# Performance work log

Hardware: AMD Instinct MI355X
Metric: run time of the kernel (lower is better)

Reference implementation:

```python
import jax, jax.numpy as jnp
import numpy as np

B, N, H = 2048, 5, 5
IN, HID, OUT = 7, 2048, 512  # IN = 1 + c + c^2 with c = (H-1)//2 = 2


def setup_inputs() -> dict:
    key = jax.random.key(0)
    ks = jax.random.split(key, 7)
    k_in = 1.0 / np.sqrt(IN).astype(np.float32)
    k_h = 1.0 / np.sqrt(HID).astype(np.float32)
    return {
        "ins": jax.random.normal(ks[0], (B, N, H, H), jnp.float32),
        "w1": (jax.random.uniform(ks[1], (4, HID, IN), jnp.float32) - 0.5) * k_in,
        "b1": (jax.random.uniform(ks[2], (HID,), jnp.float32) - 0.5) * k_in,
        "w2": (jax.random.uniform(ks[3], (4, HID, HID), jnp.float32) - 0.5) * k_h,
        "b2": (jax.random.uniform(ks[4], (HID,), jnp.float32) - 0.5) * k_h,
        "w3": (jax.random.uniform(ks[5], (4, OUT, HID), jnp.float32) - 0.5) * k_h,
        "b3": (jax.random.uniform(ks[6], (OUT,), jnp.float32) - 0.5) * k_h,
        "ln_g": jnp.ones((HID,), jnp.float32),
        "ln_b": jnp.zeros((HID,), jnp.float32),
    }


def _rot90(x):
    # matches torch: x.flip(3).permute(0,1,3,2)
    return jnp.swapaxes(jnp.flip(x, axis=3), 2, 3)


def _orbit_stack(x):
    b, n = x.shape[0], x.shape[1]
    c = (x.shape[-1] - 1) // 2  # = 2 for H=5
    center = x[:, :, c, c]  # (B,N)
    parts = []
    xi = x
    for _ in range(4):  # fixed C4 group orbit, not a data loop
        parts.append(xi[:, :, :c, :c + 1].reshape(b, n, -1))  # (B,N,c+c^2)
        xi = _rot90(xi)
    orb = jnp.stack(parts, axis=-1)  # (B,N,c+c^2,4)
    cen = jnp.broadcast_to(center[..., None, None], (b, n, 1, 4))
    out = jnp.concatenate([cen, orb], axis=2)  # (B,N,n_orbits,4)
    return jnp.transpose(out, (0, 1, 3, 2))  # (B,N,4,n_orbits)


def _c4conv(w, bias, x):
    # block-circulant kernel: mat[g,h] = w[(h-g) % 4]
    mat = jnp.stack([jnp.roll(w, i, axis=0) for i in range(4)], axis=0)  # (4,4,out,in)
    return jnp.einsum('ghij,bnhj->bngi', mat, x) + bias


def _layernorm(x, g, b, eps=1e-5):
    m = jnp.mean(x, axis=-1, keepdims=True)
    v = jnp.mean(jnp.square(x - m), axis=-1, keepdims=True)
    return (x - m) / jnp.sqrt(v + eps) * g + b


def reference(ins, w1, b1, w2, b2, w3, b3, ln_g, ln_b):
    h = _orbit_stack(ins)                          # (B,N,4,7)
    h = jax.nn.relu(_c4conv(w1, b1, h))            # (B,N,4,HID)
    h = jax.nn.relu(_layernorm(_c4conv(w2, b2, h), ln_g, ln_b))
    return _c4conv(w3, b3, h)                      # (B,N,4,OUT)
```

## Files before the change

### kernel.cpp

```cpp
#include <hip/hip_runtime.h>
#include <stdint.h>


#define HID 2048
#define MROWS 10240

typedef float floatx4 __attribute__((ext_vector_type(4)));
typedef __bf16 bf16x8 __attribute__((ext_vector_type(8)));

__device__ __forceinline__ unsigned short f2bf(float f) {
  union { float f; unsigned int u; } v; v.f = f;
  unsigned int r = v.u + 0x7fffu + ((v.u >> 16) & 1u);
  return (unsigned short)(r >> 16);
}
__device__ __forceinline__ float bf2f(unsigned short s) {
  union { unsigned int u; float f; } v; v.u = ((unsigned int)s) << 16;
  return v.f;
}

template <int NO>
__global__ __launch_bounds__(256) void wtrans_kernel(const float* __restrict__ w,
                                                     unsigned short* __restrict__ W0s,
                                                     unsigned short* __restrict__ W2s,
                                                     unsigned short* __restrict__ Bc) {
  int idx = blockIdx.x * 256 + threadIdx.x;
  int i = idx >> 9, j4 = idx & 511;
  const float4* wp = (const float4*)w;
  float4 w0 = wp[0 * NO * 512 + i * 512 + j4];
  float4 w1 = wp[1 * NO * 512 + i * 512 + j4];
  float4 w2 = wp[2 * NO * 512 + i * 512 + j4];
  float4 w3 = wp[3 * NO * 512 + i * 512 + j4];
  ushort4 s0, s2, vr, vi, nvi;
#define DO(c)                                        \
  s0.c = f2bf(w0.c + w1.c + w2.c + w3.c);            \
  s2.c = f2bf(w0.c - w1.c + w2.c - w3.c);            \
  vr.c = f2bf(w0.c - w2.c);                          \
  vi.c = f2bf(w1.c - w3.c);                          \
  nvi.c = f2bf(-(w1.c - w3.c));
  DO(x) DO(y) DO(z) DO(w)
#undef DO
  ((ushort4*)W0s)[i * 512 + j4] = s0;
  ((ushort4*)W2s)[i * 512 + j4] = s2;
  ((ushort4*)Bc)[i * 1024 + j4] = vr;
  ((ushort4*)Bc)[i * 1024 + 512 + j4] = nvi;
  ((ushort4*)Bc)[(NO + i) * 1024 + j4] = vi;
  ((ushort4*)Bc)[(NO + i) * 1024 + 512 + j4] = vr;
}

__global__ __launch_bounds__(256) void layer1_kernel(const float* __restrict__ ins,
                                                     const float* __restrict__ w1,
                                                     const float* __restrict__ b1,
                                                     unsigned short* __restrict__ h1s,
                                                     int row0) {
  __shared__ float orbs[32][28];
  int t = threadIdx.x;
  int b0 = blockIdx.x * 32;
  int i = blockIdx.y * 256 + t;
  if (t < 32) {
    const float* x = ins + (size_t)(row0 + b0 + t) * 25;
    float v[25];
#pragma unroll
    for (int p = 0; p < 25; ++p) v[p] = x[p];
    float* o = orbs[t];
    o[0] = v[12]; o[7] = v[12]; o[14] = v[12]; o[21] = v[12];
#pragma unroll
    for (int r = 0; r < 2; ++r)
#pragma unroll
      for (int c = 0; c < 3; ++c) {
        int m = 1 + r * 3 + c;
        o[m]      = v[r * 5 + c];
        o[7 + m]  = v[c * 5 + (4 - r)];
        o[14 + m] = v[(4 - r) * 5 + (4 - c)];
        o[21 + m] = v[(4 - c) * 5 + r];
      }
  }
  __syncthreads();
  float w[4][7];
#pragma unroll
  for (int r = 0; r < 4; ++r)
#pragma unroll
    for (int j = 0; j < 7; ++j) w[r][j] = w1[(r * HID + i) * 7 + j];
  float bias = b1[i];
  for (int s = 0; s < 32; ++s) {
    float a[4] = {bias, bias, bias, bias};
#pragma unroll
    for (int hh = 0; hh < 4; ++hh)
#pragma unroll
      for (int j = 0; j < 7; ++j) {
        float ov = orbs[s][hh * 7 + j];
#pragma unroll
        for (int g = 0; g < 4; ++g) a[g] += w[(hh - g) & 3][j] * ov;
      }
    float h0 = fmaxf(a[0], 0.f), h1 = fmaxf(a[1], 0.f);
    float h2 = fmaxf(a[2], 0.f), h3 = fmaxf(a[3], 0.f);
    size_t base = (size_t)(b0 + s) * 8192 + i;
    h1s[base]        = f2bf(h0 + h1 + h2 + h3);
    h1s[base + 2048] = f2bf(h0 - h1 + h2 - h3);
    h1s[base + 4096] = f2bf(h0 - h2);
    h1s[base + 6144] = f2bf(h3 - h1);
  }
}


__global__ __launch_bounds__(512, 2) void gemm_spec(const unsigned short* __restrict__ A,
                                                    const unsigned short* __restrict__ B0,
                                                    const unsigned short* __restrict__ B1,
                                                    const unsigned short* __restrict__ B2,
                                                    float* __restrict__ Cf,
                                                    unsigned short* __restrict__ Cb,
                                                    int s1, int s2, int N0, int ldc,
                                                    int NT, int NTL, int MTN) {
  __shared__ __align__(16) unsigned short As[2][16384];
  __shared__ __align__(16) unsigned short Bs[2][16384];
  int tid = threadIdx.x;
  int wave = tid >> 6, lane = tid & 63;
  int lane15 = lane & 15, lane4 = lane >> 4, l7 = lane15 & 7;
  int wm = wave >> 2, wn = wave & 3;
  int wm64 = wm << 6, wn32 = wn << 5;

  int srow = tid >> 3;
  int scol = ((tid & 7) ^ ((tid >> 3) & 7)) << 3;
  int bs64 = (srow >> 5) << 6;

#define STA(buf, mh, kk)                                                                              \
  __builtin_amdgcn_global_load_lds(                                                                   \
      (const __attribute__((address_space(1))) void*)(Agb + (size_t)((mh) * 64) * 8192 + (kk)),       \
      (__attribute__((address_space(3))) void*)((char*)As[buf] + (mh) * 16384 + wave * 1024),         \
      16, 0, 0);                                                                                      \
  __builtin_amdgcn_global_load_lds(                                                                   \
      (const __attribute__((address_space(1))) void*)(Agb + (size_t)((mh) * 64 + 128) * 8192 + (kk)), \
      (__attribute__((address_space(3))) void*)((char*)As[buf] + (mh) * 16384 + 8192 + wave * 1024),  \
      16, 0, 0)

#define STB(buf, nh, kk)                                                                              \
  __builtin_amdgcn_global_load_lds(                                                                   \
      (const __attribute__((address_space(1))) void*)(Bgb + (size_t)(bs64 + (nh) * 32) * ldb + (kk)), \
      (__attribute__((address_space(3))) void*)((char*)Bs[buf] + (nh) * 16384 + wave * 1024),         \
      16, 0, 0);                                                                                      \
  __builtin_amdgcn_global_load_lds(                                                                   \
      (const __attribute__((address_space(1))) void*)(Bgb + (size_t)(bs64 + 128 + (nh) * 32) * ldb + (kk)), \
      (__attribute__((address_space(3))) void*)((char*)Bs[buf] + (nh) * 16384 + 8192 + wave * 1024),  \
      16, 0, 0)

#define RAF(buf, mh)                                                                                  \
  _Pragma("unroll") for (int mi_ = 0; mi_ < 4; ++mi_)                                                 \
  _Pragma("unroll") for (int ks_ = 0; ks_ < 2; ++ks_)                                                 \
      af[mi_][ks_] = *(const bf16x8*)((const char*)As[buf] +                                          \
          (((mh) * 128 + wm64 + mi_ * 16 + lane15) << 7) + (((ks_ * 4 + lane4) ^ l7) << 4))

#define RBF(dst, buf, nh)                                                                             \
  _Pragma("unroll") for (int ni_ = 0; ni_ < 2; ++ni_)                                                 \
  _Pragma("unroll") for (int ks_ = 0; ks_ < 2; ++ks_)                                                 \
      dst[ni_][ks_] = *(const bf16x8*)((const char*)Bs[buf] +                                         \
          (((nh) * 128 + wn32 + ni_ * 16 + lane15) << 7) + (((ks_ * 4 + lane4) ^ l7) << 4))

#define MM(mh, nh, bF)                                                                                \
  _Pragma("unroll") for (int mi_ = 0; mi_ < 4; ++mi_)                                                 \
  _Pragma("unroll") for (int ni_ = 0; ni_ < 2; ++ni_)                                                 \
  _Pragma("unroll") for (int ks_ = 0; ks_ < 2; ++ks_)                                                 \
      acc[(mh) * 4 + mi_][(nh) * 2 + ni_] = __builtin_amdgcn_mfma_f32_16x16x32_bf16(                  \
          af[mi_][ks_], bF[ni_][ks_], acc[(mh) * 4 + mi_][(nh) * 2 + ni_], 0, 0, 0)

#define BAR() __builtin_amdgcn_s_barrier()
#define LGKM0() asm volatile("s_waitcnt lgkmcnt(0)" ::: "memory")
#define LGKM8() asm volatile("s_waitcnt lgkmcnt(8)" ::: "memory")
#define VM6() asm volatile("s_waitcnt vmcnt(6)" ::: "memory")
#define VM8() asm volatile("s_waitcnt vmcnt(8)" ::: "memory")

  bf16x8 af[4][2], b0r[2][2], b1r[2][2];
  const floatx4 fz = {0.f, 0.f, 0.f, 0.f};
  floatx4 acc[8][4];

  int G = (int)gridDim.x;
  for (int pass = 0;; ++pass) {
    int base = pass * G;
    if (base >= NT) break;
    int wt = (pass & 1) ? (base + G - 1 - (int)blockIdx.x) : (base + (int)blockIdx.x);
    if (wt >= NT) continue;

    int mt, nt;
    if (wt < NTL) { int j = wt / MTN; nt = s2 + j; mt = wt - j * MTN; }
    else          { int w2_ = wt - NTL; int j = w2_ / MTN; nt = j; mt = w2_ - j * MTN; }
    int m0 = mt * 256;

    const unsigned short* Bp;
    int K, aoff, coff, nloc;
    if (nt < s1)      { Bp = B0; K = 2048; aoff = 0;    coff = 0;      nloc = nt * 256; }
    else if (nt < s2) { Bp = B1; K = 2048; aoff = 2048; coff = N0;     nloc = (nt - s1) * 256; }
    else              { Bp = B2; K = 4096; aoff = 4096; coff = 2 * N0; nloc = (nt - s2) * 256; }
    int ldb = K;

    const unsigned short* Agb = A + (size_t)(m0 + srow) * 8192 + aoff + scol;
    const unsigned short* Bgb = Bp + (size_t)(nloc + (srow & 31)) * ldb + scol;

#pragma unroll
    for (int a = 0; a < 8; ++a)
#pragma unroll
      for (int b = 0; b < 4; ++b) acc[a][b] = fz;

    STA(0, 0, 0); STB(0, 0, 0); STB(0, 1, 0); STA(0, 1, 0);
    STA(1, 0, 64); STB(1, 0, 64); STB(1, 1, 64); STA(1, 1, 64);
    VM8();
    BAR();

    for (int k0 = 0; k0 < K; k0 += 128) {
      RAF(0, 0); RBF(b0r, 0, 0);
      LGKM8();
      BAR(); LGKM0();
      __builtin_amdgcn_s_setprio(1); MM(0, 0, b0r); __builtin_amdgcn_s_setprio(0);
      BAR();
      RBF(b1r, 0, 1);
      STA(0, 0, k0 + 128);
      BAR(); LGKM0();
      __builtin_amdgcn_s_setprio(1); MM(0, 1, b1r); __builtin_amdgcn_s_setprio(0);
      BAR();
      RAF(0, 1);
      STB(0, 0, k0 + 128);
      BAR(); LGKM0();
      __builtin_amdgcn_s_setprio(1); MM(1, 0, b0r); __builtin_amdgcn_s_setprio(0);
      BAR();
      STB(0, 1, k0 + 128);
      BAR(); LGKM0();
      __builtin_amdgcn_s_setprio(1); MM(1, 1, b1r); __builtin_amdgcn_s_setprio(0);
      VM6();
      BAR();
      RAF(1, 0); RBF(b0r, 1, 0);
      STA(0, 1, k0 + 128);
      LGKM8();
      BAR(); LGKM0();
      __builtin_amdgcn_s_setprio(1); MM(0, 0, b0r); __builtin_amdgcn_s_setprio(0);
      BAR();
      RBF(b1r, 1, 1);
      STA(1, 0, k0 + 192);
      BAR(); LGKM0();
      __builtin_amdgcn_s_setprio(1); MM(0, 1, b1r); __builtin_amdgcn_s_setprio(0);
      BAR();
      RAF(1, 1);
      STB(1, 0, k0 + 192);
      BAR(); LGKM0();
      __builtin_amdgcn_s_setprio(1); MM(1, 0, b0r); __builtin_amdgcn_s_setprio(0);
      BAR();
      STB(1, 1, k0 + 192);
      STA(1, 1, k0 + 192);
      BAR(); LGKM0();
      __builtin_amdgcn_s_setprio(1); MM(1, 1, b1r); __builtin_amdgcn_s_setprio(0);
      VM6();
      BAR();
    }
    asm volatile("s_waitcnt vmcnt(0)" ::: "memory");

#pragma unroll
    for (int ni = 0; ni < 4; ++ni) {
      int col = coff + nloc + wn * 64 + (ni >> 1) * 32 + (ni & 1) * 16 + lane15;
#pragma unroll
      for (int mi = 0; mi < 8; ++mi) {
        int row = m0 + wm * 128 + (mi >> 2) * 64 + (mi & 3) * 16 + lane4 * 4;
        if (Cb) {
#pragma unroll
          for (int r = 0; r < 4; ++r)
            __builtin_nontemporal_store(f2bf(acc[mi][ni][r]),
                                        &Cb[(size_t)(row + r) * ldc + col]);
        } else {
#pragma unroll
          for (int r = 0; r < 4; ++r)
            __builtin_nontemporal_store(acc[mi][ni][r],
                                        &Cf[(size_t)(row + r) * ldc + col]);
        }
      }
    }
  }
#undef STA
#undef STB
#undef RAF
#undef RBF
#undef MM
#undef BAR
#undef LGKM0
#undef LGKM8
#undef VM6
#undef VM8
}

__global__ __launch_bounds__(256) void ln_spec_kernel(const unsigned short* C2,
                                                      const float* __restrict__ b2,
                                                      const float* __restrict__ ln_g,
                                                      const float* __restrict__ ln_b,
                                                      unsigned short* h1s) {
  int t = threadIdx.x;
  size_t base = (size_t)blockIdx.x * 8192;
  const ushort4* p = (const ushort4*)(C2 + base);
  const float4* bp2 = (const float4*)b2;
  float4 y[4][2];
  float s[4] = {0, 0, 0, 0}, q[4] = {0, 0, 0, 0};
#pragma unroll
  for (int hl = 0; hl < 2; ++hl) {
    int j = hl * 256 + t;
    ushort4 u0 = p[j], u2 = p[512 + j], ur = p[1024 + j], ui = p[1536 + j];
    float4 bb = bp2[j];
#define DO(c)                                                   \
  {                                                             \
    float v0 = bf2f(u0.c), v2 = bf2f(u2.c);                     \
    float vr = bf2f(ur.c), vi = bf2f(ui.c);                     \
    float e0 = 0.25f * (v0 + v2 + 2.f * vr) + bb.c;             \
    float e1 = 0.25f * (v0 - v2 - 2.f * vi) + bb.c;             \
    float e2 = 0.25f * (v0 + v2 - 2.f * vr) + bb.c;             \
    float e3 = 0.25f * (v0 - v2 + 2.f * vi) + bb.c;             \
    y[0][hl].c = e0; y[1][hl].c = e1; y[2][hl].c = e2; y[3][hl].c = e3; \
    s[0] += e0; q[0] += e0 * e0; s[1] += e1; q[1] += e1 * e1;   \
    s[2] += e2; q[2] += e2 * e2; s[3] += e3; q[3] += e3 * e3;   \
  }
    DO(x) DO(y) DO(z) DO(w)
#undef DO
  }
#pragma unroll
  for (int off = 32; off > 0; off >>= 1)
#pragma unroll
    for (int g = 0; g < 4; ++g) {
      s[g] += __shfl_down(s[g], off, 64);
      q[g] += __shfl_down(q[g], off, 64);
    }
  __shared__ float rs[4][4], rq[4][4];
  int w = t >> 6, l = t & 63;
  if (l == 0)
#pragma unroll
    for (int g = 0; g < 4; ++g) { rs[w][g] = s[g]; rq[w][g] = q[g]; }
  __syncthreads();
  float mean[4], rstd[4];
#pragma unroll
  for (int g = 0; g < 4; ++g) {
    float ss = rs[0][g] + rs[1][g] + rs[2][g] + rs[3][g];
    float qq = rq[0][g] + rq[1][g] + rq[2][g] + rq[3][g];
    mean[g] = ss * (1.f / HID);
    float var = qq * (1.f / HID) - mean[g] * mean[g];
    rstd[g] = rsqrtf(var + 1e-5f);
  }
  const float4* gp = (const float4*)ln_g;
  const float4* lbp = (const float4*)ln_b;
#pragma unroll
  for (int hl = 0; hl < 2; ++hl) {
    int j = hl * 256 + t;
    float4 gg = gp[j], lb = lbp[j];
    ushort4 o[4];
#define DO(c)                                                               \
  {                                                                         \
    float h0 = fmaxf((y[0][hl].c - mean[0]) * rstd[0] * gg.c + lb.c, 0.f);  \
    float h1 = fmaxf((y[1][hl].c - mean[1]) * rstd[1] * gg.c + lb.c, 0.f);  \
    float h2 = fmaxf((y[2][hl].c - mean[2]) * rstd[2] * gg.c + lb.c, 0.f);  \
    float h3 = fmaxf((y[3][hl].c - mean[3]) * rstd[3] * gg.c + lb.c, 0.f);  \
    o[0].c = f2bf(h0 + h1 + h2 + h3);                                       \
    o[1].c = f2bf(h0 - h1 + h2 - h3);                                       \
    o[2].c = f2bf(h0 - h2);                                                 \
    o[3].c = f2bf(h3 - h1);                                                 \
  }
    DO(x) DO(y) DO(z) DO(w)
#undef DO
    size_t ob = (size_t)blockIdx.x * 8192;
#pragma unroll
    for (int pl = 0; pl < 4; ++pl)
      ((ushort4*)(h1s + ob + pl * 2048))[j] = o[pl];
  }
}

__global__ __launch_bounds__(256) void out_ep_kernel(const float* __restrict__ Z,
                                                     const float* __restrict__ b3,
                                                     float* __restrict__ out) {
  int e = blockIdx.x * 256 + threadIdx.x;
  int row = e >> 7, i4 = e & 127;
  const float4* Z4 = (const float4*)Z;
  const float4* b34 = (const float4*)b3;
  float4* o4 = (float4*)out;
  size_t base = (size_t)row * 512;
  float4 z0 = Z4[base + i4],       z2 = Z4[base + 128 + i4];
  float4 zr = Z4[base + 256 + i4], zi = Z4[base + 384 + i4];
  float4 bv = b34[i4];
  float4 e0, e1, e2, e3;
#define DO(c)                                     \
  e0.c = 0.25f * (z0.c + z2.c + 2.f * zr.c) + bv.c; \
  e1.c = 0.25f * (z0.c - z2.c - 2.f * zi.c) + bv.c; \
  e2.c = 0.25f * (z0.c + z2.c - 2.f * zr.c) + bv.c; \
  e3.c = 0.25f * (z0.c - z2.c + 2.f * zi.c) + bv.c;
  DO(x) DO(y) DO(z) DO(w)
#undef DO
  o4[base + i4]       = e0;
  o4[base + 128 + i4] = e1;
  o4[base + 256 + i4] = e2;
  o4[base + 384 + i4] = e3;
}

extern "C" void kernel_launch(void* const* d_in, const int* in_sizes, int n_in,
                              void* d_out, int out_size, void* d_ws, size_t ws_size,
                              hipStream_t stream) {
  const float* ins = (const float*)d_in[0];
  const float* w1  = (const float*)d_in[1];
  const float* b1  = (const float*)d_in[2];
  const float* w2  = (const float*)d_in[3];
  const float* b2  = (const float*)d_in[4];
  const float* w3  = (const float*)d_in[5];
  const float* b3  = (const float*)d_in[6];
  const float* lng = (const float*)d_in[7];
  const float* lnb = (const float*)d_in[8];
  float* out = (float*)d_out;
  char* ws = (char*)d_ws;

  unsigned short* W0s2 = (unsigned short*)ws;
  unsigned short* W2s2 = W0s2 + 4194304;
  unsigned short* Bc2  = W2s2 + 4194304;
  unsigned short* W0s3 = Bc2 + 16777216;
  unsigned short* W2s3 = W0s3 + 1048576;
  unsigned short* Bc3  = W2s3 + 1048576;
  const size_t WT_BYTES = 62914560ull;
  char* chunk_base = ws + WT_BYTES;

  wtrans_kernel<2048><<<4096, 256, 0, stream>>>(w2, W0s2, W2s2, Bc2);
  wtrans_kernel<512><<<1024, 256, 0, stream>>>(w3, W0s3, W2s3, Bc3);

  const size_t H1_BYTES = (size_t)5120 * 8192 * 2;
  const size_t H2_BYTES = (size_t)MROWS * 8192 * 2;
  const size_t need_full = WT_BYTES + H1_BYTES + H2_BYTES + 4096;

  if (ws_size >= need_full) {
    unsigned short* h1s = (unsigned short*)chunk_base;
    float*          Z   = (float*)chunk_base;
    unsigned short* H2  = (unsigned short*)(chunk_base + H1_BYTES);
    const int Mc = 5120, MTN = Mc / 256;
    for (int c = 0; c < 2; ++c) {
      int row0 = c * Mc;
      unsigned short* H2c = H2 + (size_t)row0 * 8192;
      layer1_kernel<<<dim3(Mc / 32, 8), 256, 0, stream>>>(ins, w1, b1, h1s, row0);
      gemm_spec<<<256, 512, 0, stream>>>(h1s, W0s2, W2s2, Bc2, nullptr, H2c,
                                         8, 16, 2048, 8192, 32 * MTN, 16 * MTN, MTN);
      ln_spec_kernel<<<Mc, 256, 0, stream>>>(H2c, b2, lng, lnb, H2c);
    }
    {
      const int MT3 = MROWS / 256;
      gemm_spec<<<256, 512, 0, stream>>>(H2, W0s3, W2s3, Bc3, Z, nullptr,
                                         2, 4, 512, 2048, 8 * MT3, 4 * MT3, MT3);
      out_ep_kernel<<<MROWS / 2, 256, 0, stream>>>(Z, b3, out);
    }
  } else {
    static const int Pcand[8] = {1, 2, 4, 5, 8, 10, 20, 40};
    int P = 40;
    for (int pi = 0; pi < 8; ++pi) {
      size_t mc = (size_t)MROWS / Pcand[pi];
      size_t need = WT_BYTES + mc * 8192 * 2 * 2 + 4096;
      if (need <= ws_size) { P = Pcand[pi]; break; }
    }
    const int Mc = MROWS / P, MTN = Mc / 256;
    unsigned short* h1s = (unsigned short*)chunk_base;
    unsigned short* C2  = (unsigned short*)(chunk_base + (size_t)Mc * 8192 * 2);
    float*          Z   = (float*)C2;
    for (int c = 0; c < P; ++c) {
      int row0 = c * Mc;
      layer1_kernel<<<dim3(Mc / 32, 8), 256, 0, stream>>>(ins, w1, b1, h1s, row0);
      gemm_spec<<<256, 512, 0, stream>>>(h1s, W0s2, W2s2, Bc2, nullptr, C2,
                                         8, 16, 2048, 8192, 32 * MTN, 16 * MTN, MTN);
      ln_spec_kernel<<<Mc, 256, 0, stream>>>(C2, b2, lng, lnb, h1s);
      gemm_spec<<<256, 512, 0, stream>>>(h1s, W0s3, W2s3, Bc3, Z, nullptr,
                                         2, 4, 512, 2048, 8 * MTN, 4 * MTN, MTN);
      out_ep_kernel<<<Mc / 2, 256, 0, stream>>>(Z, b3, out + (size_t)row0 * 2048);
    }
  }
}
```

Baseline: 1.107 ms.

## Use Karatsuba-style complex product to cut C4 spectral GEMM work

The complex-frequency block of each C4 conv was a K=4096 real GEMM. It now uses three K=2048 real products (vr, vi, vr+vi) via a Karatsuba-style trick, and the real and imaginary parts are rebuilt in the LN and output epilogues. This cuts the FLOPs of the complex part from 4 to 3 real products, at the cost of a wider activation layout (AW=10240) and an extra stored plane. It also simplifies GEMM tile scheduling into uniform K=2048 segments, drops nontemporal stores, and switches the row chunking to 6144/4096 with layer 3 run per chunk.

```diff
diff --git a/kernel.cpp b/kernel.cpp
--- a/kernel.cpp
+++ b/kernel.cpp
@@ -4,6 +4,7 @@
 
 #define HID 2048
 #define MROWS 10240
+#define AW 10240
 
 typedef float floatx4 __attribute__((ext_vector_type(4)));
 typedef __bf16 bf16x8 __attribute__((ext_vector_type(8)));
@@ -20,9 +21,7 @@
 
 template <int NO>
 __global__ __launch_bounds__(256) void wtrans_kernel(const float* __restrict__ w,
-                                                     unsigned short* __restrict__ W0s,
-                                                     unsigned short* __restrict__ W2s,
-                                                     unsigned short* __restrict__ Bc) {
+                                                     unsigned short* __restrict__ Wb) {
   int idx = blockIdx.x * 256 + threadIdx.x;
   int i = idx >> 9, j4 = idx & 511;
   const float4* wp = (const float4*)w;
@@ -30,21 +29,25 @@
   float4 w1 = wp[1 * NO * 512 + i * 512 + j4];
   float4 w2 = wp[2 * NO * 512 + i * 512 + j4];
   float4 w3 = wp[3 * NO * 512 + i * 512 + j4];
-  ushort4 s0, s2, vr, vi, nvi;
+  ushort4 s0, s2, vr, vi, vs;
 #define DO(c)                                        \
-  s0.c = f2bf(w0.c + w1.c + w2.c + w3.c);            \
-  s2.c = f2bf(w0.c - w1.c + w2.c - w3.c);            \
-  vr.c = f2bf(w0.c - w2.c);                          \
-  vi.c = f2bf(w1.c - w3.c);                          \
-  nvi.c = f2bf(-(w1.c - w3.c));
+  {                                                  \
+    float vrf = w0.c - w2.c, vif = w1.c - w3.c;      \
+    s0.c = f2bf(w0.c + w1.c + w2.c + w3.c);          \
+    s2.c = f2bf(w0.c - w1.c + w2.c - w3.c);          \
+    vr.c = f2bf(vrf);                                \
+    vi.c = f2bf(vif);                                \
+    vs.c = f2bf(vrf + vif);                          \
+  }
   DO(x) DO(y) DO(z) DO(w)
 #undef DO
-  ((ushort4*)W0s)[i * 512 + j4] = s0;
-  ((ushort4*)W2s)[i * 512 + j4] = s2;
-  ((ushort4*)Bc)[i * 1024 + j4] = vr;
-  ((ushort4*)Bc)[i * 1024 + 512 + j4] = nvi;
-  ((ushort4*)Bc)[(NO + i) * 1024 + j4] = vi;
-  ((ushort4*)Bc)[(NO + i) * 1024 + 512 + j4] = vr;
+  ushort4* O = (ushort4*)Wb;
+  const int MS = NO * 512;
+  O[0 * MS + i * 512 + j4] = s0;
+  O[1 * MS + i * 512 + j4] = s2;
+  O[2 * MS + i * 512 + j4] = vr;
+  O[3 * MS + i * 512 + j4] = vi;
+  O[4 * MS + i * 512 + j4] = vs;
 }
 
 __global__ __launch_bounds__(256) void layer1_kernel(const float* __restrict__ ins,
@@ -93,23 +96,23 @@
       }
     float h0 = fmaxf(a[0], 0.f), h1 = fmaxf(a[1], 0.f);
     float h2 = fmaxf(a[2], 0.f), h3 = fmaxf(a[3], 0.f);
-    size_t base = (size_t)(b0 + s) * 8192 + i;
+    float ur = h0 - h2, ui = h3 - h1;
+    size_t base = (size_t)(b0 + s) * AW + i;
     h1s[base]        = f2bf(h0 + h1 + h2 + h3);
     h1s[base + 2048] = f2bf(h0 - h1 + h2 - h3);
-    h1s[base + 4096] = f2bf(h0 - h2);
-    h1s[base + 6144] = f2bf(h3 - h1);
+    h1s[base + 4096] = f2bf(ur);
+    h1s[base + 6144] = f2bf(ui);
+    h1s[base + 8192] = f2bf(ur + ui);
   }
 }
 
 
 __global__ __launch_bounds__(512, 2) void gemm_spec(const unsigned short* __restrict__ A,
-                                                    const unsigned short* __restrict__ B0,
-                                                    const unsigned short* __restrict__ B1,
-                                                    const unsigned short* __restrict__ B2,
+                                                    const unsigned short* __restrict__ Bb,
                                                     float* __restrict__ Cf,
                                                     unsigned short* __restrict__ Cb,
-                                                    int s1, int s2, int N0, int ldc,
-                                                    int NT, int NTL, int MTN) {
+                                                    int N0, int ldc,
+                                                    int NT, int MTN, int segN) {
   __shared__ __align__(16) unsigned short As[2][16384];
   __shared__ __align__(16) unsigned short Bs[2][16384];
   int tid = threadIdx.x;
@@ -121,14 +124,15 @@
   int srow = tid >> 3;
   int scol = ((tid & 7) ^ ((tid >> 3) & 7)) << 3;
   int bs64 = (srow >> 5) << 6;
+  const int K = 2048, ldb = 2048;
 
 #define STA(buf, mh, kk)                                                                              \
   __builtin_amdgcn_global_load_lds(                                                                   \
-      (const __attribute__((address_space(1))) void*)(Agb + (size_t)((mh) * 64) * 8192 + (kk)),       \
+      (const __attribute__((address_space(1))) void*)(Agb + (size_t)((mh) * 64) * AW + (kk)),         \
       (__attribute__((address_space(3))) void*)((char*)As[buf] + (mh) * 16384 + wave * 1024),         \
       16, 0, 0);                                                                                      \
   __builtin_amdgcn_global_load_lds(                                                                   \
-      (const __attribute__((address_space(1))) void*)(Agb + (size_t)((mh) * 64 + 128) * 8192 + (kk)), \
+      (const __attribute__((address_space(1))) void*)(Agb + (size_t)((mh) * 64 + 128) * AW + (kk)),   \
       (__attribute__((address_space(3))) void*)((char*)As[buf] + (mh) * 16384 + 8192 + wave * 1024),  \
       16, 0, 0)
 
@@ -178,19 +182,13 @@
     int wt = (pass & 1) ? (base + G - 1 - (int)blockIdx.x) : (base + (int)blockIdx.x);
     if (wt >= NT) continue;
 
-    int mt, nt;
-    if (wt < NTL) { int j = wt / MTN; nt = s2 + j; mt = wt - j * MTN; }
-    else          { int w2_ = wt - NTL; int j = w2_ / MTN; nt = j; mt = w2_ - j * MTN; }
+    int nt = wt / MTN, mt = wt - nt * MTN;
     int m0 = mt * 256;
-
-    const unsigned short* Bp;
-    int K, aoff, coff, nloc;
-    if (nt < s1)      { Bp = B0; K = 2048; aoff = 0;    coff = 0;      nloc = nt * 256; }
-    else if (nt < s2) { Bp = B1; K = 2048; aoff = 2048; coff = N0;     nloc = (nt - s1) * 256; }
-    else              { Bp = B2; K = 4096; aoff = 4096; coff = 2 * N0; nloc = (nt - s2) * 256; }
-    int ldb = K;
-
-    const unsigned short* Agb = A + (size_t)(m0 + srow) * 8192 + aoff + scol;
+    int seg = nt / segN, nloc = (nt - seg * segN) * 256;
+    const unsigned short* Bp = Bb + (size_t)seg * N0 * 2048;
+    int aoff = seg * 2048, coff = seg * N0;
+
+    const unsigned short* Agb = A + (size_t)(m0 + srow) * AW + aoff + scol;
     const unsigned short* Bgb = Bp + (size_t)(nloc + (srow & 31)) * ldb + scol;
 
 #pragma unroll
@@ -204,44 +202,46 @@
     BAR();
 
     for (int k0 = 0; k0 < K; k0 += 128) {
+      int ka = k0 + 128; if (ka >= K) ka = 0;
+      int kb = k0 + 192; if (kb >= K) kb = 0;
       RAF(0, 0); RBF(b0r, 0, 0);
       LGKM8();
       BAR(); LGKM0();
       __builtin_amdgcn_s_setprio(1); MM(0, 0, b0r); __builtin_amdgcn_s_setprio(0);
       BAR();
       RBF(b1r, 0, 1);
-      STA(0, 0, k0 + 128);
+      STA(0, 0, ka);
       BAR(); LGKM0();
       __builtin_amdgcn_s_setprio(1); MM(0, 1, b1r); __builtin_amdgcn_s_setprio(0);
       BAR();
       RAF(0, 1);
-      STB(0, 0, k0 + 128);
+      STB(0, 0, ka);
       BAR(); LGKM0();
       __builtin_amdgcn_s_setprio(1); MM(1, 0, b0r); __builtin_amdgcn_s_setprio(0);
       BAR();
-      STB(0, 1, k0 + 128);
+      STB(0, 1, ka);
       BAR(); LGKM0();
       __builtin_amdgcn_s_setprio(1); MM(1, 1, b1r); __builtin_amdgcn_s_setprio(0);
       VM6();
       BAR();
       RAF(1, 0); RBF(b0r, 1, 0);
-      STA(0, 1, k0 + 128);
+      STA(0, 1, ka);
       LGKM8();
       BAR(); LGKM0();
       __builtin_amdgcn_s_setprio(1); MM(0, 0, b0r); __builtin_amdgcn_s_setprio(0);
       BAR();
       RBF(b1r, 1, 1);
-      STA(1, 0, k0 + 192);
+      STA(1, 0, kb);
       BAR(); LGKM0();
       __builtin_amdgcn_s_setprio(1); MM(0, 1, b1r); __builtin_amdgcn_s_setprio(0);
       BAR();
       RAF(1, 1);
-      STB(1, 0, k0 + 192);
+      STB(1, 0, kb);
       BAR(); LGKM0();
       __builtin_amdgcn_s_setprio(1); MM(1, 0, b0r); __builtin_amdgcn_s_setprio(0);
       BAR();
-      STB(1, 1, k0 + 192);
-      STA(1, 1, k0 + 192);
+      STB(1, 1, kb);
+      STA(1, 1, kb);
       BAR(); LGKM0();
       __builtin_amdgcn_s_setprio(1); MM(1, 1, b1r); __builtin_amdgcn_s_setprio(0);
       VM6();
@@ -258,13 +258,11 @@
         if (Cb) {
 #pragma unroll
           for (int r = 0; r < 4; ++r)
-            __builtin_nontemporal_store(f2bf(acc[mi][ni][r]),
-                                        &Cb[(size_t)(row + r) * ldc + col]);
+            Cb[(size_t)(row + r) * ldc + col] = f2bf(acc[mi][ni][r]);
         } else {
 #pragma unroll
           for (int r = 0; r < 4; ++r)
-            __builtin_nontemporal_store(acc[mi][ni][r],
-                                        &Cf[(size_t)(row + r) * ldc + col]);
+            Cf[(size_t)(row + r) * ldc + col] = acc[mi][ni][r];
         }
       }
     }
@@ -287,7 +285,7 @@
                                                       const float* __restrict__ ln_b,
                                                       unsigned short* h1s) {
   int t = threadIdx.x;
-  size_t base = (size_t)blockIdx.x * 8192;
+  size_t base = (size_t)blockIdx.x * AW;
   const ushort4* p = (const ushort4*)(C2 + base);
   const float4* bp2 = (const float4*)b2;
   float4 y[4][2];
@@ -295,12 +293,14 @@
 #pragma unroll
   for (int hl = 0; hl < 2; ++hl) {
     int j = hl * 256 + t;
-    ushort4 u0 = p[j], u2 = p[512 + j], ur = p[1024 + j], ui = p[1536 + j];
+    ushort4 u0 = p[j], u2 = p[512 + j];
+    ushort4 t1 = p[1024 + j], t2v = p[1536 + j], t3 = p[2048 + j];
     float4 bb = bp2[j];
 #define DO(c)                                                   \
   {                                                             \
     float v0 = bf2f(u0.c), v2 = bf2f(u2.c);                     \
-    float vr = bf2f(ur.c), vi = bf2f(ui.c);                     \
+    float T1 = bf2f(t1.c), T2 = bf2f(t2v.c), T3 = bf2f(t3.c);   \
+    float vr = T1 - T2, vi = T3 - T1 - T2;                      \
     float e0 = 0.25f * (v0 + v2 + 2.f * vr) + bb.c;             \
     float e1 = 0.25f * (v0 - v2 - 2.f * vi) + bb.c;             \
     float e2 = 0.25f * (v0 + v2 - 2.f * vr) + bb.c;             \
@@ -340,24 +340,26 @@
   for (int hl = 0; hl < 2; ++hl) {
     int j = hl * 256 + t;
     float4 gg = gp[j], lb = lbp[j];
-    ushort4 o[4];
+    ushort4 o[5];
 #define DO(c)                                                               \
   {                                                                         \
     float h0 = fmaxf((y[0][hl].c - mean[0]) * rstd[0] * gg.c + lb.c, 0.f);  \
     float h1 = fmaxf((y[1][hl].c - mean[1]) * rstd[1] * gg.c + lb.c, 0.f);  \
     float h2 = fmaxf((y[2][hl].c - mean[2]) * rstd[2] * gg.c + lb.c, 0.f);  \
     float h3 = fmaxf((y[3][hl].c - mean[3]) * rstd[3] * gg.c + lb.c, 0.f);  \
+    float our = h0 - h2, oui = h3 - h1;                                     \
     o[0].c = f2bf(h0 + h1 + h2 + h3);                                       \
     o[1].c = f2bf(h0 - h1 + h2 - h3);                                       \
-    o[2].c = f2bf(h0 - h2);                                                 \
-    o[3].c = f2bf(h3 - h1);                                                 \
+    o[2].c = f2bf(our);                                                     \
+    o[3].c = f2bf(oui);                                                     \
+    o[4].c = f2bf(our + oui);                                               \
   }
     DO(x) DO(y) DO(z) DO(w)
 #undef DO
-    size_t ob = (size_t)blockIdx.x * 8192;
-#pragma unroll
-    for (int pl = 0; pl < 4; ++pl)
-      ((ushort4*)(h1s + ob + pl * 2048))[j] = o[pl];
+    unsigned short* hp = h1s + base;
+#pragma unroll
+    for (int pl = 0; pl < 5; ++pl)
+      ((ushort4*)hp)[pl * 512 + j] = o[pl];
   }
 }
 
@@ -369,22 +371,25 @@
   const float4* Z4 = (const float4*)Z;
   const float4* b34 = (const float4*)b3;
   float4* o4 = (float4*)out;
-  size_t base = (size_t)row * 512;
-  float4 z0 = Z4[base + i4],       z2 = Z4[base + 128 + i4];
-  float4 zr = Z4[base + 256 + i4], zi = Z4[base + 384 + i4];
+  size_t zb = (size_t)row * 640, ob = (size_t)row * 512;
+  float4 z0 = Z4[zb + i4],       z2 = Z4[zb + 128 + i4];
+  float4 T1 = Z4[zb + 256 + i4], T2 = Z4[zb + 384 + i4], T3 = Z4[zb + 512 + i4];
   float4 bv = b34[i4];
   float4 e0, e1, e2, e3;
-#define DO(c)                                     \
-  e0.c = 0.25f * (z0.c + z2.c + 2.f * zr.c) + bv.c; \
-  e1.c = 0.25f * (z0.c - z2.c - 2.f * zi.c) + bv.c; \
-  e2.c = 0.25f * (z0.c + z2.c - 2.f * zr.c) + bv.c; \
-  e3.c = 0.25f * (z0.c - z2.c + 2.f * zi.c) + bv.c;
+#define DO(c)                                       \
+  {                                                 \
+    float zr = T1.c - T2.c, zi = T3.c - T1.c - T2.c; \
+    e0.c = 0.25f * (z0.c + z2.c + 2.f * zr) + bv.c;  \
+    e1.c = 0.25f * (z0.c - z2.c - 2.f * zi) + bv.c;  \
+    e2.c = 0.25f * (z0.c + z2.c - 2.f * zr) + bv.c;  \
+    e3.c = 0.25f * (z0.c - z2.c + 2.f * zi) + bv.c;  \
+  }
   DO(x) DO(y) DO(z) DO(w)
 #undef DO
-  o4[base + i4]       = e0;
-  o4[base + 128 + i4] = e1;
-  o4[base + 256 + i4] = e2;
-  o4[base + 384 + i4] = e3;
+  o4[ob + i4]       = e0;
+  o4[ob + 128 + i4] = e1;
+  o4[ob + 256 + i4] = e2;
+  o4[ob + 384 + i4] = e3;
 }
 
 extern "C" void kernel_launch(void* const* d_in, const int* in_sizes, int n_in,
@@ -402,62 +407,46 @@
   float* out = (float*)d_out;
   char* ws = (char*)d_ws;
 
-  unsigned short* W0s2 = (unsigned short*)ws;
-  unsigned short* W2s2 = W0s2 + 4194304;
-  unsigned short* Bc2  = W2s2 + 4194304;
-  unsigned short* W0s3 = Bc2 + 16777216;
-  unsigned short* W2s3 = W0s3 + 1048576;
-  unsigned short* Bc3  = W2s3 + 1048576;
-  const size_t WT_BYTES = 62914560ull;
+  unsigned short* Wb2 = (unsigned short*)ws;
+  unsigned short* Wb3 = Wb2 + 5u * 2048 * 2048;
+  const size_t WT_BYTES = (5ull * 2048 * 2048 + 5ull * 512 * 2048) * 2;
   char* chunk_base = ws + WT_BYTES;
 
-  wtrans_kernel<2048><<<4096, 256, 0, stream>>>(w2, W0s2, W2s2, Bc2);
-  wtrans_kernel<512><<<1024, 256, 0, stream>>>(w3, W0s3, W2s3, Bc3);
-
-  const size_t H1_BYTES = (size_t)5120 * 8192 * 2;
-  const size_t H2_BYTES = (size_t)MROWS * 8192 * 2;
-  const size_t need_full = WT_BYTES + H1_BYTES + H2_BYTES + 4096;
-
-  if (ws_size >= need_full) {
-    unsigned short* h1s = (unsigned short*)chunk_base;
-    float*          Z   = (float*)chunk_base;
-    unsigned short* H2  = (unsigned short*)(chunk_base + H1_BYTES);
-    const int Mc = 5120, MTN = Mc / 256;
+  wtrans_kernel<2048><<<4096, 256, 0, stream>>>(w2, Wb2);
+  wtrans_kernel<512><<<1024, 256, 0, stream>>>(w3, Wb3);
+
+  const size_t H1MAX = (size_t)6144 * AW * 2;
+  const size_t need = WT_BYTES + 2 * H1MAX + 4096;
+
+  unsigned short* h1s = (unsigned short*)chunk_base;
+  unsigned short* H2  = (unsigned short*)(chunk_base + H1MAX);
+  float*          Z   = (float*)chunk_base;
+
+  if (ws_size >= need) {
+    const int r0s[2] = {0, 6144};
+    const int mcs[2] = {6144, 4096};
     for (int c = 0; c < 2; ++c) {
-      int row0 = c * Mc;
-      unsigned short* H2c = H2 + (size_t)row0 * 8192;
+      int row0 = r0s[c], Mc = mcs[c], MTN = Mc / 256;
       layer1_kernel<<<dim3(Mc / 32, 8), 256, 0, stream>>>(ins, w1, b1, h1s, row0);
-      gemm_spec<<<256, 512, 0, stream>>>(h1s, W0s2, W2s2, Bc2, nullptr, H2c,
-                                         8, 16, 2048, 8192, 32 * MTN, 16 * MTN, MTN);
-      ln_spec_kernel<<<Mc, 256, 0, stream>>>(H2c, b2, lng, lnb, H2c);
-    }
-    {
-      const int MT3 = MROWS / 256;
-      gemm_spec<<<256, 512, 0, stream>>>(H2, W0s3, W2s3, Bc3, Z, nullptr,
-                                         2, 4, 512, 2048, 8 * MT3, 4 * MT3, MT3);
-      out_ep_kernel<<<MROWS / 2, 256, 0, stream>>>(Z, b3, out);
+      gemm_spec<<<256, 512, 0, stream>>>(h1s, Wb2, nullptr, H2,
+                                         2048, AW, 40 * MTN, MTN, 8);
+      ln_spec_kernel<<<Mc, 256, 0, stream>>>(H2, b2, lng, lnb, H2);
+      gemm_spec<<<256, 512, 0, stream>>>(H2, Wb3, Z, nullptr,
+                                         512, 2560, 10 * MTN, MTN, 2);
+      out_ep_kernel<<<Mc / 2, 256, 0, stream>>>(Z, b3, out + (size_t)row0 * 2048);
     }
   } else {
-    static const int Pcand[8] = {1, 2, 4, 5, 8, 10, 20, 40};
-    int P = 40;
-    for (int pi = 0; pi < 8; ++pi) {
-      size_t mc = (size_t)MROWS / Pcand[pi];
-      size_t need = WT_BYTES + mc * 8192 * 2 * 2 + 4096;
-      if (need <= ws_size) { P = Pcand[pi]; break; }
+    for (int c = 0; c < 5; ++c) {
+      int row0 = c * 2048, Mc = 2048, MTN = 8;
+      unsigned short* H2c = (unsigned short*)(chunk_base + (size_t)Mc * AW * 2);
+      float* Zc = (float*)chunk_base;
+      layer1_kernel<<<dim3(Mc / 32, 8), 256, 0, stream>>>(ins, w1, b1, h1s, row0);
+      gemm_spec<<<256, 512, 0, stream>>>(h1s, Wb2, nullptr, H2c,
+                                         2048, AW, 40 * MTN, MTN, 8);
+      ln_spec_kernel<<<Mc, 256, 0, stream>>>(H2c, b2, lng, lnb, H2c);
+      gemm_spec<<<256, 512, 0, stream>>>(H2c, Wb3, Zc, nullptr,
+                                         512, 2560, 10 * MTN, MTN, 2);
+      out_ep_kernel<<<Mc / 2, 256, 0, stream>>>(Zc, b3, out + (size_t)row0 * 2048);
     }
-    const int Mc = MROWS / P, MTN = Mc / 256;
-    unsigned short* h1s = (unsigned short*)chunk_base;
-    unsigned short* C2  = (unsigned short*)(chunk_base + (size_t)Mc * 8192 * 2);
-    float*          Z   = (float*)C2;
-    for (int c = 0; c < P; ++c) {
-      int row0 = c * Mc;
-      layer1_kernel<<<dim3(Mc / 32, 8), 256, 0, stream>>>(ins, w1, b1, h1s, row0);
-      gemm_spec<<<256, 512, 0, stream>>>(h1s, W0s2, W2s2, Bc2, nullptr, C2,
-                                         8, 16, 2048, 8192, 32 * MTN, 16 * MTN, MTN);
-      ln_spec_kernel<<<Mc, 256, 0, stream>>>(C2, b2, lng, lnb, h1s);
-      gemm_spec<<<256, 512, 0, stream>>>(h1s, W0s3, W2s3, Bc3, Z, nullptr,
-                                         2, 4, 512, 2048, 8 * MTN, 4 * MTN, MTN);
-      out_ep_kernel<<<Mc / 2, 256, 0, stream>>>(Z, b3, out + (size_t)row0 * 2048);
-    }
-  }
-}
+  }
+}
```

Result: faster. 1.003 ms (-9.4%).
